# Performance work log

Measured on AMD Instinct MI355X. Metric: run time of the kernel, lower is better.

## Reference

```python
import jax, jax.numpy as jnp
import numpy as np

LEVELS = 8
DB2 = [0.4829629131445341, 0.8365163037378079, 0.22414386804185735, -0.12940952255092145]


def make_wavelet(h):
    # g = flip(h); g[1::2] *= -1  (torch compute_wavelet)
    g = jnp.flip(h, -1)
    sign = jnp.where(jnp.arange(g.shape[-1]) % 2 == 0, 1.0, -1.0).astype(g.dtype)
    return g * sign


def circ_conv(x, f, tr=False):
    # FFT-based circular convolution, output length == input length (NORM='backward').
    L = x.shape[-1]
    F = jnp.fft.rfft(f, n=L)
    if tr:
        F = jnp.conj(F)  # circular correlation for the synthesis side
    return jnp.fft.irfft(jnp.fft.rfft(x, n=L) * F, n=L)


def despawn_forward(x, scaling):
    levels = scaling.shape[0]
    L = x.shape[1]
    D = 2 ** int(np.ceil(np.log2(L)))
    pl = (D - L) // 2
    pr = int(np.ceil((D - L) / 2))
    x = jnp.pad(x, ((0, 0), (pl, pr)), mode='edge')  # ReplicationPad1d

    # Analysis: per-level circular filter + dyadic downsample
    approx = x
    details_list = []
    for lev in range(levels):
        h = scaling[lev]
        g = make_wavelet(h)
        d = circ_conv(approx, g)[:, ::2]
        approx = circ_conv(approx, h)[:, ::2]
        details_list.append(d)
    coeffs = details_list + [approx]

    # Synthesis: zero-insert upsample + circular correlation (no thresholding,
    # matching the original forward which never applies HardThreshold)
    rec = approx
    for lev in reversed(range(levels)):
        h = scaling[lev]
        g = make_wavelet(h)
        d = details_list[lev]
        n, m = d.shape
        ud = jnp.zeros((n, 2 * m), d.dtype).at[:, ::2].set(d)
        ua = jnp.zeros((n, 2 * m), rec.dtype).at[:, ::2].set(rec)
        rec = circ_conv(ud, g, tr=True) + circ_conv(ua, h, tr=True)

    return rec[:, pl:L + pr], jnp.concatenate(coeffs, axis=-1)


def setup_inputs() -> dict:
    key = jax.random.key(0)
    k1, _ = jax.random.split(key)
    x = jax.random.normal(k1, (2048, 8192), dtype=jnp.float32)
    scaling = jnp.tile(jnp.asarray(DB2, dtype=jnp.float32), (LEVELS, 1))  # (levels, 4)
    return {"x": x, "scaling": scaling}


def reference(x, scaling):
    return despawn_forward(x, scaling)
```

## Files before the change

### kernel.cpp

```cpp
#include <hip/hip_runtime.h>

#define COLS   8192
#define LEVELS 8
#define TPB    512

typedef float f4_t __attribute__((ext_vector_type(4)));

__device__ __forceinline__ void nt_store4(float* p, const float4 v) {
    f4_t w; w.x = v.x; w.y = v.y; w.z = v.z; w.w = v.w;
    __builtin_nontemporal_store(w, reinterpret_cast<f4_t*>(p));
}

__device__ __forceinline__ void bar_lds() {
    asm volatile("s_waitcnt lgkmcnt(0)" ::: "memory");
    __builtin_amdgcn_sched_barrier(0);
    __builtin_amdgcn_s_barrier();
    __builtin_amdgcn_sched_barrier(0);
}

__global__ __launch_bounds__(TPB, 8) void despawn_kernel(
    const float* __restrict__ x, const float* __restrict__ scaling,
    float* __restrict__ out, int rows)
{
    __shared__ __align__(16) float B[COLS / 2];
    __shared__ __align__(16) float C[COLS / 4];
    __shared__ __align__(16) float D[COLS / 4];
    __shared__ float filt[LEVELS * 4];

    const int row = blockIdx.x;
    const int tid = threadIdx.x;

    if (tid < LEVELS * 4) filt[tid] = scaling[tid];
    bar_lds();

    const float* __restrict__ xg       = x + (size_t)row * COLS;
    float* __restrict__       out_rec  = out + (size_t)row * COLS;
    float* __restrict__       out_coef = out + (size_t)rows * COLS + (size_t)row * COLS;

    {
        const float h0 = filt[0], h1 = filt[1], h2 = filt[2], h3 = filt[3];
        const float g0 = h3, g1 = -h2, g2 = h1, g3 = -h0;
        const float4* __restrict__ xg4 = reinterpret_cast<const float4*>(xg);
        const int q8 = COLS / 8, qm = COLS / 4 - 1;
        for (int i = tid; i < q8; i += TPB) {
            const float4 va = xg4[(2 * i - 1) & qm];
            const float4 vb = xg4[2 * i];
            const float4 vc = xg4[2 * i + 1];
            float4 dv, av;
            dv.x = g0*vb.x + g1*va.w + g2*va.z + g3*va.y;
            av.x = h0*vb.x + h1*va.w + h2*va.z + h3*va.y;
            dv.y = g0*vb.z + g1*vb.y + g2*vb.x + g3*va.w;
            av.y = h0*vb.z + h1*vb.y + h2*vb.x + h3*va.w;
            dv.z = g0*vc.x + g1*vb.w + g2*vb.z + g3*vb.y;
            av.z = h0*vc.x + h1*vb.w + h2*vb.z + h3*vb.y;
            dv.w = g0*vc.z + g1*vc.y + g2*vc.x + g3*vb.w;
            av.w = h0*vc.z + h1*vc.y + h2*vc.x + h3*vb.w;
            reinterpret_cast<float4*>(out_coef)[i] = dv;
            reinterpret_cast<float4*>(B)[i]        = av;
        }
        bar_lds();
    }

    int n = COLS / 2, coff = COLS / 2, dOff = 0;
    float* cur = B;
    float* nxt = C;
    for (int lev = 1; lev <= 3; ++lev) {
        const float h0 = filt[4*lev+0], h1 = filt[4*lev+1],
                    h2 = filt[4*lev+2], h3 = filt[4*lev+3];
        const float g0 = h3, g1 = -h2, g2 = h1, g3 = -h0;
        const int half = n >> 1, qq = half >> 2, qm = (n >> 2) - 1;
        const float4* c4 = reinterpret_cast<const float4*>(cur);
        float* ob = out_coef + coff;
        float4* n4 = reinterpret_cast<float4*>(nxt);
        float4* D4 = reinterpret_cast<float4*>(D + dOff);
        const bool toD = (lev >= 2);
        for (int p = tid; p < qq; p += TPB) {
            const float4 va = c4[(2 * p - 1) & qm];
            const float4 vb = c4[2 * p];
            const float4 vc = c4[2 * p + 1];
            float4 dv, av;
            dv.x = g0*vb.x + g1*va.w + g2*va.z + g3*va.y;
            av.x = h0*vb.x + h1*va.w + h2*va.z + h3*va.y;
            dv.y = g0*vb.z + g1*vb.y + g2*vb.x + g3*va.w;
            av.y = h0*vb.z + h1*vb.y + h2*vb.x + h3*va.w;
            dv.z = g0*vc.x + g1*vb.w + g2*vb.z + g3*vb.y;
            av.z = h0*vc.x + h1*vb.w + h2*vb.z + h3*vb.y;
            dv.w = g0*vc.z + g1*vc.y + g2*vc.x + g3*vb.w;
            av.w = h0*vc.z + h1*vc.y + h2*vc.x + h3*vb.w;
            if (toD) {
                nt_store4(ob + 4*p, dv);
                D4[p] = dv;
            } else {
                reinterpret_cast<float4*>(ob)[p] = dv;
            }
            n4[p] = av;
        }
        bar_lds();
        coff += half;
        if (toD) dOff += half;
        n = half;
        float* t = cur; cur = nxt; nxt = t;
    }

    if (tid < 64) {
        float* acur = C;
        float* anxt = B;
        int nn = 512, coffW = 7680, dW = 1536;
        for (int lev = 4; lev <= 7; ++lev) {
            const float h0 = filt[4*lev+0], h1 = filt[4*lev+1],
                        h2 = filt[4*lev+2], h3 = filt[4*lev+3];
            const float g0 = h3, g1 = -h2, g2 = h1, g3 = -h0;
            const int half = nn >> 1, mask = nn - 1;
            for (int i = tid; i < half; i += 64) {
                const int b = 2 * i;
                const float x0 = acur[b];
                const float x1 = acur[(b - 1) & mask];
                const float x2 = acur[(b - 2) & mask];
                const float x3 = acur[(b - 3) & mask];
                const float d = g0*x0 + g1*x1 + g2*x2 + g3*x3;
                const float a = h0*x0 + h1*x1 + h2*x2 + h3*x3;
                D[dW + i] = d;
                __builtin_nontemporal_store(d, &out_coef[coffW + i]);
                if (lev == 7) {
                    D[2016 + i] = a;
                    __builtin_nontemporal_store(a, &out_coef[8160 + i]);
                }
                else          anxt[i] = a;
            }
            __builtin_amdgcn_wave_barrier();
            coffW += half; dW += half; nn = half;
            float* t = acur; acur = anxt; anxt = t;
        }
        int mS = 32, dS = 1984;
        const float* aprevW = D + 2016;
        for (int lev = 7; lev >= 4; --lev) {
            const float h0 = filt[4*lev+0], h1 = filt[4*lev+1],
                        h2 = filt[4*lev+2], h3 = filt[4*lev+3];
            const float g0 = h3, g1 = -h2, g2 = h1, g3 = -h0;
            const int mm = mS - 1;
            float* recW = (lev & 1) ? B : C;
            for (int j = tid; j < mS; j += 64) {
                const float dj  = D[dS + j];
                const float dj1 = D[dS + ((j + 1) & mm)];
                const float dj2 = D[dS + ((j + 2) & mm)];
                const float aj  = aprevW[j];
                const float aj1 = aprevW[(j + 1) & mm];
                const float aj2 = aprevW[(j + 2) & mm];
                recW[2*j]     = g0*dj  + g2*dj1 + h0*aj  + h2*aj1;
                recW[2*j + 1] = g1*dj1 + g3*dj2 + h1*aj1 + h3*aj2;
            }
            __builtin_amdgcn_wave_barrier();
            aprevW = recW; mS <<= 1; dS -= mS;
        }
    }
    __syncthreads();

#define SYNTH_BODY(d2)                                                        \
    for (int p = tid; p < mp; p += TPB) {                                     \
        const float2 dv0 = (d2)[p];                                           \
        const float2 dv1 = (d2)[(p + 1) & mm];                                \
        const float2 av0 = a2[p];                                             \
        const float2 av1 = a2[(p + 1) & mm];                                  \
        const float r0 = g0*dv0.x + g2*dv0.y + h0*av0.x + h2*av0.y;           \
        const float r1 = g1*dv0.y + g3*dv1.x + h1*av0.y + h3*av1.x;           \
        const float r2 = g0*dv0.y + g2*dv1.x + h0*av0.y + h2*av1.x;           \
        const float r3 = g1*dv1.x + g3*dv1.y + h1*av1.x + h3*av1.y;           \
        const float4 rv = make_float4(r0, r1, r2, r3);                        \
        if (last) nt_store4(out_rec + 4*p, rv);                               \
        else      reinterpret_cast<float4*>(rec)[p] = rv;                     \
    }

    const float* aprev = C;
    int m = 512;
    for (int lev = 3; lev >= 0; --lev) {
        const float h0 = filt[4*lev+0], h1 = filt[4*lev+1],
                    h2 = filt[4*lev+2], h3 = filt[4*lev+3];
        const float g0 = h3, g1 = -h2, g2 = h1, g3 = -h0;
        const int mp = m >> 1, mm = mp - 1;
        const float2* a2 = reinterpret_cast<const float2*>(aprev);
        float* rec = (lev & 1) ? B : C;
        const bool last = (lev == 0);
        if (lev >= 2) {
            const float2* dL = reinterpret_cast<const float2*>(D + ((lev == 3) ? 1024 : 0));
            SYNTH_BODY(dL)
        } else {
            const float2* __restrict__ dG =
                reinterpret_cast<const float2*>(out_coef + ((lev == 1) ? 4096 : 0));
            SYNTH_BODY(dG)
        }
        if (lev) bar_lds();
        aprev = rec; m <<= 1;
    }
#undef SYNTH_BODY
}

extern "C" void kernel_launch(void* const* d_in, const int* in_sizes, int n_in,
                              void* d_out, int out_size, void* d_ws, size_t ws_size,
                              hipStream_t stream) {
    const float* x       = (const float*)d_in[0];
    const float* scaling = (const float*)d_in[1];
    float* out           = (float*)d_out;
    const int rows = in_sizes[0] / COLS;
    despawn_kernel<<<rows, TPB, 0, stream>>>(x, scaling, out, rows);
}
```

Measured before the change: 42.20 us.

## Process two rows per block and run the serial deep levels on parallel waves

Each block now handles two rows, with the shared buffers doubled per row and the grid halved. The serial single-wave stage for levels 4-7 now runs on two waves at once, one per row, so the idle tail per block is spread over more work and the barrier count per row is halved. In exchange LDS use per block doubles, the occupancy hint drops from 8 to 4, and fewer blocks are launched (1024 instead of 2048). The launch also assumes the row count is even.

```diff
diff --git a/kernel.cpp b/kernel.cpp
--- a/kernel.cpp
+++ b/kernel.cpp
@@ -3,6 +3,7 @@
 #define COLS   8192
 #define LEVELS 8
 #define TPB    512
+#define RPB    2
 
 typedef float f4_t __attribute__((ext_vector_type(4)));
 
@@ -18,180 +19,195 @@
     __builtin_amdgcn_sched_barrier(0);
 }
 
-__global__ __launch_bounds__(TPB, 8) void despawn_kernel(
+__global__ __launch_bounds__(TPB, 4) void despawn_kernel(
     const float* __restrict__ x, const float* __restrict__ scaling,
     float* __restrict__ out, int rows)
 {
-    __shared__ __align__(16) float B[COLS / 2];
-    __shared__ __align__(16) float C[COLS / 4];
-    __shared__ __align__(16) float D[COLS / 4];
+    __shared__ __align__(16) float B[RPB][4096];
+    __shared__ __align__(16) float C[RPB][2048];
+    __shared__ __align__(16) float D[RPB][2048];
     __shared__ float filt[LEVELS * 4];
 
-    const int row = blockIdx.x;
     const int tid = threadIdx.x;
-
     if (tid < LEVELS * 4) filt[tid] = scaling[tid];
     bar_lds();
 
-    const float* __restrict__ xg       = x + (size_t)row * COLS;
-    float* __restrict__       out_rec  = out + (size_t)row * COLS;
-    float* __restrict__       out_coef = out + (size_t)rows * COLS + (size_t)row * COLS;
+    const size_t row0 = (size_t)blockIdx.x * RPB;
+    const size_t cbase = (size_t)rows * COLS;
 
     {
         const float h0 = filt[0], h1 = filt[1], h2 = filt[2], h3 = filt[3];
         const float g0 = h3, g1 = -h2, g2 = h1, g3 = -h0;
-        const float4* __restrict__ xg4 = reinterpret_cast<const float4*>(xg);
         const int q8 = COLS / 8, qm = COLS / 4 - 1;
-        for (int i = tid; i < q8; i += TPB) {
-            const float4 va = xg4[(2 * i - 1) & qm];
-            const float4 vb = xg4[2 * i];
-            const float4 vc = xg4[2 * i + 1];
-            float4 dv, av;
-            dv.x = g0*vb.x + g1*va.w + g2*va.z + g3*va.y;
-            av.x = h0*vb.x + h1*va.w + h2*va.z + h3*va.y;
-            dv.y = g0*vb.z + g1*vb.y + g2*vb.x + g3*va.w;
-            av.y = h0*vb.z + h1*vb.y + h2*vb.x + h3*va.w;
-            dv.z = g0*vc.x + g1*vb.w + g2*vb.z + g3*vb.y;
-            av.z = h0*vc.x + h1*vb.w + h2*vb.z + h3*vb.y;
-            dv.w = g0*vc.z + g1*vc.y + g2*vc.x + g3*vb.w;
-            av.w = h0*vc.z + h1*vc.y + h2*vc.x + h3*vb.w;
-            reinterpret_cast<float4*>(out_coef)[i] = dv;
-            reinterpret_cast<float4*>(B)[i]        = av;
+        #pragma unroll
+        for (int r = 0; r < RPB; ++r) {
+            const float4* __restrict__ xg4 =
+                reinterpret_cast<const float4*>(x + (row0 + r) * COLS);
+            float* __restrict__ oc = out + cbase + (row0 + r) * COLS;
+            for (int i = tid; i < q8; i += TPB) {
+                const float4 va = xg4[(2 * i - 1) & qm];
+                const float4 vb = xg4[2 * i];
+                const float4 vc = xg4[2 * i + 1];
+                float4 dv, av;
+                dv.x = g0*vb.x + g1*va.w + g2*va.z + g3*va.y;
+                av.x = h0*vb.x + h1*va.w + h2*va.z + h3*va.y;
+                dv.y = g0*vb.z + g1*vb.y + g2*vb.x + g3*va.w;
+                av.y = h0*vb.z + h1*vb.y + h2*vb.x + h3*va.w;
+                dv.z = g0*vc.x + g1*vb.w + g2*vb.z + g3*vb.y;
+                av.z = h0*vc.x + h1*vb.w + h2*vb.z + h3*vb.y;
+                dv.w = g0*vc.z + g1*vc.y + g2*vc.x + g3*vb.w;
+                av.w = h0*vc.z + h1*vc.y + h2*vc.x + h3*vb.w;
+                reinterpret_cast<float4*>(oc)[i]   = dv;
+                reinterpret_cast<float4*>(B[r])[i] = av;
+            }
         }
         bar_lds();
     }
 
-    int n = COLS / 2, coff = COLS / 2, dOff = 0;
-    float* cur = B;
-    float* nxt = C;
-    for (int lev = 1; lev <= 3; ++lev) {
-        const float h0 = filt[4*lev+0], h1 = filt[4*lev+1],
-                    h2 = filt[4*lev+2], h3 = filt[4*lev+3];
-        const float g0 = h3, g1 = -h2, g2 = h1, g3 = -h0;
-        const int half = n >> 1, qq = half >> 2, qm = (n >> 2) - 1;
-        const float4* c4 = reinterpret_cast<const float4*>(cur);
-        float* ob = out_coef + coff;
-        float4* n4 = reinterpret_cast<float4*>(nxt);
-        float4* D4 = reinterpret_cast<float4*>(D + dOff);
-        const bool toD = (lev >= 2);
-        for (int p = tid; p < qq; p += TPB) {
-            const float4 va = c4[(2 * p - 1) & qm];
-            const float4 vb = c4[2 * p];
-            const float4 vc = c4[2 * p + 1];
-            float4 dv, av;
-            dv.x = g0*vb.x + g1*va.w + g2*va.z + g3*va.y;
-            av.x = h0*vb.x + h1*va.w + h2*va.z + h3*va.y;
-            dv.y = g0*vb.z + g1*vb.y + g2*vb.x + g3*va.w;
-            av.y = h0*vb.z + h1*vb.y + h2*vb.x + h3*va.w;
-            dv.z = g0*vc.x + g1*vb.w + g2*vb.z + g3*vb.y;
-            av.z = h0*vc.x + h1*vb.w + h2*vb.z + h3*vb.y;
-            dv.w = g0*vc.z + g1*vc.y + g2*vc.x + g3*vb.w;
-            av.w = h0*vc.z + h1*vc.y + h2*vc.x + h3*vb.w;
-            if (toD) {
-                nt_store4(ob + 4*p, dv);
-                D4[p] = dv;
-            } else {
-                reinterpret_cast<float4*>(ob)[p] = dv;
-            }
-            n4[p] = av;
-        }
-        bar_lds();
-        coff += half;
-        if (toD) dOff += half;
-        n = half;
-        float* t = cur; cur = nxt; nxt = t;
-    }
-
-    if (tid < 64) {
-        float* acur = C;
-        float* anxt = B;
-        int nn = 512, coffW = 7680, dW = 1536;
-        for (int lev = 4; lev <= 7; ++lev) {
+    {
+        int n = COLS / 2, coff = COLS / 2, dOff = 0;
+        float* cur[RPB] = { B[0], B[1] };
+        float* nxt[RPB] = { C[0], C[1] };
+        for (int lev = 1; lev <= 3; ++lev) {
             const float h0 = filt[4*lev+0], h1 = filt[4*lev+1],
                         h2 = filt[4*lev+2], h3 = filt[4*lev+3];
             const float g0 = h3, g1 = -h2, g2 = h1, g3 = -h0;
-            const int half = nn >> 1, mask = nn - 1;
-            for (int i = tid; i < half; i += 64) {
-                const int b = 2 * i;
-                const float x0 = acur[b];
-                const float x1 = acur[(b - 1) & mask];
-                const float x2 = acur[(b - 2) & mask];
-                const float x3 = acur[(b - 3) & mask];
-                const float d = g0*x0 + g1*x1 + g2*x2 + g3*x3;
-                const float a = h0*x0 + h1*x1 + h2*x2 + h3*x3;
-                D[dW + i] = d;
-                __builtin_nontemporal_store(d, &out_coef[coffW + i]);
-                if (lev == 7) {
-                    D[2016 + i] = a;
-                    __builtin_nontemporal_store(a, &out_coef[8160 + i]);
-                }
-                else          anxt[i] = a;
-            }
-            __builtin_amdgcn_wave_barrier();
-            coffW += half; dW += half; nn = half;
-            float* t = acur; acur = anxt; anxt = t;
-        }
-        int mS = 32, dS = 1984;
-        const float* aprevW = D + 2016;
-        for (int lev = 7; lev >= 4; --lev) {
+            const int half = n >> 1, qq = half >> 2, qm = (n >> 2) - 1;
+            const bool toD = (lev >= 2);
+            #pragma unroll
+            for (int r = 0; r < RPB; ++r) {
+                const float4* c4 = reinterpret_cast<const float4*>(cur[r]);
+                float* ob = out + cbase + (row0 + r) * COLS + coff;
+                float4* n4 = reinterpret_cast<float4*>(nxt[r]);
+                float4* D4 = reinterpret_cast<float4*>(D[r] + dOff);
+                for (int p = tid; p < qq; p += TPB) {
+                    const float4 va = c4[(2 * p - 1) & qm];
+                    const float4 vb = c4[2 * p];
+                    const float4 vc = c4[2 * p + 1];
+                    float4 dv, av;
+                    dv.x = g0*vb.x + g1*va.w + g2*va.z + g3*va.y;
+                    av.x = h0*vb.x + h1*va.w + h2*va.z + h3*va.y;
+                    dv.y = g0*vb.z + g1*vb.y + g2*vb.x + g3*va.w;
+                    av.y = h0*vb.z + h1*vb.y + h2*vb.x + h3*va.w;
+                    dv.z = g0*vc.x + g1*vb.w + g2*vb.z + g3*vb.y;
+                    av.z = h0*vc.x + h1*vb.w + h2*vb.z + h3*vb.y;
+                    dv.w = g0*vc.z + g1*vc.y + g2*vc.x + g3*vb.w;
+                    av.w = h0*vc.z + h1*vc.y + h2*vc.x + h3*vb.w;
+                    if (toD) {
+                        nt_store4(ob + 4*p, dv);
+                        D4[p] = dv;
+                    } else {
+                        reinterpret_cast<float4*>(ob)[p] = dv;
+                    }
+                    n4[p] = av;
+                }
+            }
+            bar_lds();
+            coff += half;
+            if (toD) dOff += half;
+            n = half;
+            #pragma unroll
+            for (int r = 0; r < RPB; ++r) { float* t = cur[r]; cur[r] = nxt[r]; nxt[r] = t; }
+        }
+    }
+
+    {
+        const int w = tid >> 6, lane = tid & 63;
+        if (w < RPB) {
+            const int r = w;
+            float* Br = B[r]; float* Cr = C[r]; float* Dr = D[r];
+            float* __restrict__ oc = out + cbase + (row0 + r) * COLS;
+            float* acur = Cr;
+            float* anxt = Br;
+            int nn = 512, coffW = 7680, dW = 1536;
+            for (int lev = 4; lev <= 7; ++lev) {
+                const float h0 = filt[4*lev+0], h1 = filt[4*lev+1],
+                            h2 = filt[4*lev+2], h3 = filt[4*lev+3];
+                const float g0 = h3, g1 = -h2, g2 = h1, g3 = -h0;
+                const int half = nn >> 1, mask = nn - 1;
+                for (int i = lane; i < half; i += 64) {
+                    const int b = 2 * i;
+                    const float x0 = acur[b];
+                    const float x1 = acur[(b - 1) & mask];
+                    const float x2 = acur[(b - 2) & mask];
+                    const float x3 = acur[(b - 3) & mask];
+                    const float d = g0*x0 + g1*x1 + g2*x2 + g3*x3;
+                    const float a = h0*x0 + h1*x1 + h2*x2 + h3*x3;
+                    Dr[dW + i] = d;
+                    __builtin_nontemporal_store(d, &oc[coffW + i]);
+                    if (lev == 7) {
+                        Dr[2016 + i] = a;
+                        __builtin_nontemporal_store(a, &oc[8160 + i]);
+                    }
+                    else anxt[i] = a;
+                }
+                __builtin_amdgcn_wave_barrier();
+                coffW += half; dW += half; nn = half;
+                float* t = acur; acur = anxt; anxt = t;
+            }
+            int mS = 32, dS = 1984;
+            const float* aprevW = Dr + 2016;
+            for (int lev = 7; lev >= 4; --lev) {
+                const float h0 = filt[4*lev+0], h1 = filt[4*lev+1],
+                            h2 = filt[4*lev+2], h3 = filt[4*lev+3];
+                const float g0 = h3, g1 = -h2, g2 = h1, g3 = -h0;
+                const int mm = mS - 1;
+                float* recW = (lev & 1) ? Br : Cr;
+                for (int j = lane; j < mS; j += 64) {
+                    const float dj  = Dr[dS + j];
+                    const float dj1 = Dr[dS + ((j + 1) & mm)];
+                    const float dj2 = Dr[dS + ((j + 2) & mm)];
+                    const float aj  = aprevW[j];
+                    const float aj1 = aprevW[(j + 1) & mm];
+                    const float aj2 = aprevW[(j + 2) & mm];
+                    recW[2*j]     = g0*dj  + g2*dj1 + h0*aj  + h2*aj1;
+                    recW[2*j + 1] = g1*dj1 + g3*dj2 + h1*aj1 + h3*aj2;
+                }
+                __builtin_amdgcn_wave_barrier();
+                aprevW = recW; mS <<= 1; dS -= mS;
+            }
+        }
+    }
+    __syncthreads();
+
+    {
+        const float* aprev[RPB] = { C[0], C[1] };
+        int m = 512;
+        for (int lev = 3; lev >= 0; --lev) {
             const float h0 = filt[4*lev+0], h1 = filt[4*lev+1],
                         h2 = filt[4*lev+2], h3 = filt[4*lev+3];
             const float g0 = h3, g1 = -h2, g2 = h1, g3 = -h0;
-            const int mm = mS - 1;
-            float* recW = (lev & 1) ? B : C;
-            for (int j = tid; j < mS; j += 64) {
-                const float dj  = D[dS + j];
-                const float dj1 = D[dS + ((j + 1) & mm)];
-                const float dj2 = D[dS + ((j + 2) & mm)];
-                const float aj  = aprevW[j];
-                const float aj1 = aprevW[(j + 1) & mm];
-                const float aj2 = aprevW[(j + 2) & mm];
-                recW[2*j]     = g0*dj  + g2*dj1 + h0*aj  + h2*aj1;
-                recW[2*j + 1] = g1*dj1 + g3*dj2 + h1*aj1 + h3*aj2;
-            }
-            __builtin_amdgcn_wave_barrier();
-            aprevW = recW; mS <<= 1; dS -= mS;
-        }
-    }
-    __syncthreads();
-
-#define SYNTH_BODY(d2)                                                        \
-    for (int p = tid; p < mp; p += TPB) {                                     \
-        const float2 dv0 = (d2)[p];                                           \
-        const float2 dv1 = (d2)[(p + 1) & mm];                                \
-        const float2 av0 = a2[p];                                             \
-        const float2 av1 = a2[(p + 1) & mm];                                  \
-        const float r0 = g0*dv0.x + g2*dv0.y + h0*av0.x + h2*av0.y;           \
-        const float r1 = g1*dv0.y + g3*dv1.x + h1*av0.y + h3*av1.x;           \
-        const float r2 = g0*dv0.y + g2*dv1.x + h0*av0.y + h2*av1.x;           \
-        const float r3 = g1*dv1.x + g3*dv1.y + h1*av1.x + h3*av1.y;           \
-        const float4 rv = make_float4(r0, r1, r2, r3);                        \
-        if (last) nt_store4(out_rec + 4*p, rv);                               \
-        else      reinterpret_cast<float4*>(rec)[p] = rv;                     \
-    }
-
-    const float* aprev = C;
-    int m = 512;
-    for (int lev = 3; lev >= 0; --lev) {
-        const float h0 = filt[4*lev+0], h1 = filt[4*lev+1],
-                    h2 = filt[4*lev+2], h3 = filt[4*lev+3];
-        const float g0 = h3, g1 = -h2, g2 = h1, g3 = -h0;
-        const int mp = m >> 1, mm = mp - 1;
-        const float2* a2 = reinterpret_cast<const float2*>(aprev);
-        float* rec = (lev & 1) ? B : C;
-        const bool last = (lev == 0);
-        if (lev >= 2) {
-            const float2* dL = reinterpret_cast<const float2*>(D + ((lev == 3) ? 1024 : 0));
-            SYNTH_BODY(dL)
-        } else {
-            const float2* __restrict__ dG =
-                reinterpret_cast<const float2*>(out_coef + ((lev == 1) ? 4096 : 0));
-            SYNTH_BODY(dG)
-        }
-        if (lev) bar_lds();
-        aprev = rec; m <<= 1;
-    }
-#undef SYNTH_BODY
+            const int mp = m >> 1, mm = mp - 1;
+            const bool last = (lev == 0);
+            #pragma unroll
+            for (int r = 0; r < RPB; ++r) {
+                const float2* a2 = reinterpret_cast<const float2*>(aprev[r]);
+                float* rec = (lev & 1) ? B[r] : C[r];
+                const float2* __restrict__ d2 =
+                    (lev >= 2)
+                    ? reinterpret_cast<const float2*>(D[r] + ((lev == 3) ? 1024 : 0))
+                    : reinterpret_cast<const float2*>(out + cbase + (row0 + r) * COLS
+                                                      + ((lev == 1) ? 4096 : 0));
+                float* __restrict__ orc = out + (row0 + r) * COLS;
+                for (int p = tid; p < mp; p += TPB) {
+                    const float2 dv0 = d2[p];
+                    const float2 dv1 = d2[(p + 1) & mm];
+                    const float2 av0 = a2[p];
+                    const float2 av1 = a2[(p + 1) & mm];
+                    const float r0 = g0*dv0.x + g2*dv0.y + h0*av0.x + h2*av0.y;
+                    const float r1 = g1*dv0.y + g3*dv1.x + h1*av0.y + h3*av1.x;
+                    const float r2 = g0*dv0.y + g2*dv1.x + h0*av0.y + h2*av1.x;
+                    const float r3 = g1*dv1.x + g3*dv1.y + h1*av1.x + h3*av1.y;
+                    const float4 rv = make_float4(r0, r1, r2, r3);
+                    if (last) nt_store4(orc + 4*p, rv);
+                    else      reinterpret_cast<float4*>(rec)[p] = rv;
+                }
+                aprev[r] = rec;
+            }
+            if (lev) bar_lds();
+            m <<= 1;
+        }
+    }
 }
 
 extern "C" void kernel_launch(void* const* d_in, const int* in_sizes, int n_in,
@@ -201,5 +217,5 @@
     const float* scaling = (const float*)d_in[1];
     float* out           = (float*)d_out;
     const int rows = in_sizes[0] / COLS;
-    despawn_kernel<<<rows, TPB, 0, stream>>>(x, scaling, out, rows);
-}
+    despawn_kernel<<<rows / RPB, TPB, 0, stream>>>(x, scaling, out, rows);
+}
```

Result: slower. 47.02 us (+11.4%).

## Keep deep wavelet levels in registers with wave shuffles and cache level-1 details in LDS

Applied to the files above, without the earlier changes.

The serial single-wave tail for levels 4-7 (analysis and synthesis) now runs from registers. Each lane holds 8 contiguous samples, and neighbour values are exchanged with __shfl instead of going through LDS with wave barriers. Level-1 detail coefficients are also stored in a new 16KB LDS buffer F, so synthesis level 1 reads them from LDS instead of global memory. Shared memory grows to about 46KB and the occupancy hint is dropped from launch bounds, which lowers the number of resident blocks per CU and may reduce latency hiding.

```diff
diff --git a/kernel.cpp b/kernel.cpp
--- a/kernel.cpp
+++ b/kernel.cpp
@@ -5,10 +5,15 @@
 #define TPB    512
 
 typedef float f4_t __attribute__((ext_vector_type(4)));
+typedef float f2_t __attribute__((ext_vector_type(2)));
 
 __device__ __forceinline__ void nt_store4(float* p, const float4 v) {
     f4_t w; w.x = v.x; w.y = v.y; w.z = v.z; w.w = v.w;
     __builtin_nontemporal_store(w, reinterpret_cast<f4_t*>(p));
+}
+__device__ __forceinline__ void nt_store2(float* p, float a, float b) {
+    f2_t w; w.x = a; w.y = b;
+    __builtin_nontemporal_store(w, reinterpret_cast<f2_t*>(p));
 }
 
 __device__ __forceinline__ void bar_lds() {
@@ -18,13 +23,51 @@
     __builtin_amdgcn_sched_barrier(0);
 }
 
-__global__ __launch_bounds__(TPB, 8) void despawn_kernel(
+#define ANA_LEVEL(CIN, ain, aout, dout, F0, F1, F2, F3)                       \
+    {                                                                         \
+        const int _src = (l - 1) & 63;                                        \
+        const float _m1 = __shfl(ain[(CIN)-1], _src);                         \
+        const float _m2 = __shfl(ain[(CIN)-2], _src);                         \
+        const float _m3 = __shfl(ain[(CIN)-3], _src);                         \
+        dout[0] = (F3)*ain[0] - (F2)*_m1 + (F1)*_m2 - (F0)*_m3;               \
+        aout[0] = (F0)*ain[0] + (F1)*_m1 + (F2)*_m2 + (F3)*_m3;               \
+        dout[1] = (F3)*ain[2] - (F2)*ain[1] + (F1)*ain[0] - (F0)*_m1;         \
+        aout[1] = (F0)*ain[2] + (F1)*ain[1] + (F2)*ain[0] + (F3)*_m1;         \
+        _Pragma("unroll")                                                     \
+        for (int _j = 2; _j < (CIN)/2; ++_j) {                                \
+            dout[_j] = (F3)*ain[2*_j] - (F2)*ain[2*_j-1] + (F1)*ain[2*_j-2] - (F0)*ain[2*_j-3]; \
+            aout[_j] = (F0)*ain[2*_j] + (F1)*ain[2*_j-1] + (F2)*ain[2*_j-2] + (F3)*ain[2*_j-3]; \
+        }                                                                     \
+    }
+
+#define SYN_LEVEL(CD, din, ain, rout, F0, F1, F2, F3)                         \
+    {                                                                         \
+        const int _src = (l + 1) & 63;                                        \
+        const float _d0 = __shfl(din[0], _src);                               \
+        const float _d1 = __shfl(din[1], _src);                               \
+        const float _a0 = __shfl(ain[0], _src);                               \
+        const float _a1 = __shfl(ain[1], _src);                               \
+        _Pragma("unroll")                                                     \
+        for (int _j = 0; _j < (CD); ++_j) {                                   \
+            const float dj  = din[_j];                                        \
+            const float dj1 = (_j+1 < (CD)) ? din[_j+1] : _d0;                \
+            const float dj2 = (_j+2 < (CD)) ? din[_j+2] : ((_j+1 < (CD)) ? _d0 : _d1); \
+            const float aj  = ain[_j];                                        \
+            const float aj1 = (_j+1 < (CD)) ? ain[_j+1] : _a0;                \
+            const float aj2 = (_j+2 < (CD)) ? ain[_j+2] : ((_j+1 < (CD)) ? _a0 : _a1); \
+            rout[2*_j]   = (F3)*dj + (F1)*dj1 + (F0)*aj + (F2)*aj1;           \
+            rout[2*_j+1] = -(F2)*dj1 - (F0)*dj2 + (F1)*aj1 + (F3)*aj2;        \
+        }                                                                     \
+    }
+
+__global__ __launch_bounds__(TPB) void despawn_kernel(
     const float* __restrict__ x, const float* __restrict__ scaling,
     float* __restrict__ out, int rows)
 {
-    __shared__ __align__(16) float B[COLS / 2];
-    __shared__ __align__(16) float C[COLS / 4];
-    __shared__ __align__(16) float D[COLS / 4];
+    __shared__ __align__(16) float B[4096];
+    __shared__ __align__(16) float C[2048];
+    __shared__ __align__(16) float D[1536];
+    __shared__ __align__(16) float F[4096];
     __shared__ float filt[LEVELS * 4];
 
     const int row = blockIdx.x;
@@ -61,97 +104,112 @@
         bar_lds();
     }
 
-    int n = COLS / 2, coff = COLS / 2, dOff = 0;
-    float* cur = B;
-    float* nxt = C;
-    for (int lev = 1; lev <= 3; ++lev) {
-        const float h0 = filt[4*lev+0], h1 = filt[4*lev+1],
-                    h2 = filt[4*lev+2], h3 = filt[4*lev+3];
-        const float g0 = h3, g1 = -h2, g2 = h1, g3 = -h0;
-        const int half = n >> 1, qq = half >> 2, qm = (n >> 2) - 1;
-        const float4* c4 = reinterpret_cast<const float4*>(cur);
-        float* ob = out_coef + coff;
-        float4* n4 = reinterpret_cast<float4*>(nxt);
-        float4* D4 = reinterpret_cast<float4*>(D + dOff);
-        const bool toD = (lev >= 2);
-        for (int p = tid; p < qq; p += TPB) {
-            const float4 va = c4[(2 * p - 1) & qm];
-            const float4 vb = c4[2 * p];
-            const float4 vc = c4[2 * p + 1];
-            float4 dv, av;
-            dv.x = g0*vb.x + g1*va.w + g2*va.z + g3*va.y;
-            av.x = h0*vb.x + h1*va.w + h2*va.z + h3*va.y;
-            dv.y = g0*vb.z + g1*vb.y + g2*vb.x + g3*va.w;
-            av.y = h0*vb.z + h1*vb.y + h2*vb.x + h3*va.w;
-            dv.z = g0*vc.x + g1*vb.w + g2*vb.z + g3*vb.y;
-            av.z = h0*vc.x + h1*vb.w + h2*vb.z + h3*vb.y;
-            dv.w = g0*vc.z + g1*vc.y + g2*vc.x + g3*vb.w;
-            av.w = h0*vc.z + h1*vc.y + h2*vc.x + h3*vb.w;
-            if (toD) {
-                nt_store4(ob + 4*p, dv);
-                D4[p] = dv;
-            } else {
-                reinterpret_cast<float4*>(ob)[p] = dv;
-            }
-            n4[p] = av;
-        }
-        bar_lds();
-        coff += half;
-        if (toD) dOff += half;
-        n = half;
-        float* t = cur; cur = nxt; nxt = t;
-    }
-
-    if (tid < 64) {
-        float* acur = C;
-        float* anxt = B;
-        int nn = 512, coffW = 7680, dW = 1536;
-        for (int lev = 4; lev <= 7; ++lev) {
+    {
+        int n = COLS / 2, coff = COLS / 2, dOff = 0;
+        float* cur = B;
+        float* nxt = C;
+        for (int lev = 1; lev <= 3; ++lev) {
             const float h0 = filt[4*lev+0], h1 = filt[4*lev+1],
                         h2 = filt[4*lev+2], h3 = filt[4*lev+3];
             const float g0 = h3, g1 = -h2, g2 = h1, g3 = -h0;
-            const int half = nn >> 1, mask = nn - 1;
-            for (int i = tid; i < half; i += 64) {
-                const int b = 2 * i;
-                const float x0 = acur[b];
-                const float x1 = acur[(b - 1) & mask];
-                const float x2 = acur[(b - 2) & mask];
-                const float x3 = acur[(b - 3) & mask];
-                const float d = g0*x0 + g1*x1 + g2*x2 + g3*x3;
-                const float a = h0*x0 + h1*x1 + h2*x2 + h3*x3;
-                D[dW + i] = d;
-                __builtin_nontemporal_store(d, &out_coef[coffW + i]);
-                if (lev == 7) {
-                    D[2016 + i] = a;
-                    __builtin_nontemporal_store(a, &out_coef[8160 + i]);
-                }
-                else          anxt[i] = a;
+            const int half = n >> 1, qq = half >> 2, qm = (n >> 2) - 1;
+            const float4* c4 = reinterpret_cast<const float4*>(cur);
+            float* ob = out_coef + coff;
+            float4* n4 = reinterpret_cast<float4*>(nxt);
+            float4* L4 = (lev == 1) ? reinterpret_cast<float4*>(F)
+                                    : reinterpret_cast<float4*>(D + dOff);
+            for (int p = tid; p < qq; p += TPB) {
+                const float4 va = c4[(2 * p - 1) & qm];
+                const float4 vb = c4[2 * p];
+                const float4 vc = c4[2 * p + 1];
+                float4 dv, av;
+                dv.x = g0*vb.x + g1*va.w + g2*va.z + g3*va.y;
+                av.x = h0*vb.x + h1*va.w + h2*va.z + h3*va.y;
+                dv.y = g0*vb.z + g1*vb.y + g2*vb.x + g3*va.w;
+                av.y = h0*vb.z + h1*vb.y + h2*vb.x + h3*va.w;
+                dv.z = g0*vc.x + g1*vb.w + g2*vb.z + g3*vb.y;
+                av.z = h0*vc.x + h1*vb.w + h2*vb.z + h3*vb.y;
+                dv.w = g0*vc.z + g1*vc.y + g2*vc.x + g3*vb.w;
+                av.w = h0*vc.z + h1*vc.y + h2*vc.x + h3*vb.w;
+                nt_store4(ob + 4*p, dv);
+                L4[p] = dv;
+                n4[p] = av;
             }
-            __builtin_amdgcn_wave_barrier();
-            coffW += half; dW += half; nn = half;
-            float* t = acur; acur = anxt; anxt = t;
-        }
-        int mS = 32, dS = 1984;
-        const float* aprevW = D + 2016;
-        for (int lev = 7; lev >= 4; --lev) {
-            const float h0 = filt[4*lev+0], h1 = filt[4*lev+1],
-                        h2 = filt[4*lev+2], h3 = filt[4*lev+3];
-            const float g0 = h3, g1 = -h2, g2 = h1, g3 = -h0;
-            const int mm = mS - 1;
-            float* recW = (lev & 1) ? B : C;
-            for (int j = tid; j < mS; j += 64) {
-                const float dj  = D[dS + j];
-                const float dj1 = D[dS + ((j + 1) & mm)];
-                const float dj2 = D[dS + ((j + 2) & mm)];
-                const float aj  = aprevW[j];
-                const float aj1 = aprevW[(j + 1) & mm];
-                const float aj2 = aprevW[(j + 2) & mm];
-                recW[2*j]     = g0*dj  + g2*dj1 + h0*aj  + h2*aj1;
-                recW[2*j + 1] = g1*dj1 + g3*dj2 + h1*aj1 + h3*aj2;
-            }
-            __builtin_amdgcn_wave_barrier();
-            aprevW = recW; mS <<= 1; dS -= mS;
-        }
+            bar_lds();
+            coff += half;
+            if (lev >= 2) dOff += half;
+            n = half;
+            float* t = cur; cur = nxt; nxt = t;
+        }
+    }
+
+    if (tid < 64) {
+        const int l = tid;
+        float a3r[8];
+        {
+            const float4 v0 = reinterpret_cast<const float4*>(C)[2*l];
+            const float4 v1 = reinterpret_cast<const float4*>(C)[2*l+1];
+            a3r[0]=v0.x; a3r[1]=v0.y; a3r[2]=v0.z; a3r[3]=v0.w;
+            a3r[4]=v1.x; a3r[5]=v1.y; a3r[6]=v1.z; a3r[7]=v1.w;
+        }
+        float a4r[4], d4r[4];
+        ANA_LEVEL(8, a3r, a4r, d4r, filt[16], filt[17], filt[18], filt[19]);
+        float a5r[2], d5r[2];
+        ANA_LEVEL(4, a4r, a5r, d5r, filt[20], filt[21], filt[22], filt[23]);
+        float a6r, d6r;
+        {
+            const float F0=filt[24],F1=filt[25],F2=filt[26],F3=filt[27];
+            const int s1 = (l-1)&63, s2 = (l-2)&63;
+            const float x0 = a5r[0];
+            const float x1 = __shfl(a5r[1], s1);
+            const float x2 = __shfl(a5r[0], s1);
+            const float x3 = __shfl(a5r[1], s2);
+            d6r = F3*x0 - F2*x1 + F1*x2 - F0*x3;
+            a6r = F0*x0 + F1*x1 + F2*x2 + F3*x3;
+        }
+        float d7r, apr;
+        {
+            const float F0=filt[28],F1=filt[29],F2=filt[30],F3=filt[31];
+            const int i2 = 2*l;
+            const float x0 = __shfl(a6r, i2 & 63);
+            const float x1 = __shfl(a6r, (i2-1)&63);
+            const float x2 = __shfl(a6r, (i2-2)&63);
+            const float x3 = __shfl(a6r, (i2-3)&63);
+            d7r = F3*x0 - F2*x1 + F1*x2 - F0*x3;
+            apr = F0*x0 + F1*x1 + F2*x2 + F3*x3;
+        }
+        nt_store4(out_coef + 7680 + 4*l, make_float4(d4r[0],d4r[1],d4r[2],d4r[3]));
+        nt_store2(out_coef + 7936 + 2*l, d5r[0], d5r[1]);
+        __builtin_nontemporal_store(d6r, &out_coef[8064 + l]);
+        if (l < 32) {
+            __builtin_nontemporal_store(d7r, &out_coef[8128 + l]);
+            __builtin_nontemporal_store(apr, &out_coef[8160 + l]);
+        }
+        float rec7;
+        {
+            const float F0=filt[28],F1=filt[29],F2=filt[30],F3=filt[31];
+            const float dj = d7r, dj1 = __shfl(d7r,(l+1)&31), dj2 = __shfl(d7r,(l+2)&31);
+            const float aj = apr, aj1 = __shfl(apr,(l+1)&31), aj2 = __shfl(apr,(l+2)&31);
+            const float r0 = F3*dj + F1*dj1 + F0*aj + F2*aj1;
+            const float r1 = -F2*dj1 - F0*dj2 + F1*aj1 + F3*aj2;
+            const float e0 = __shfl(r0, l>>1);
+            const float e1 = __shfl(r1, l>>1);
+            rec7 = (l & 1) ? e1 : e0;
+        }
+        float rec6[2];
+        {
+            const float F0=filt[24],F1=filt[25],F2=filt[26],F3=filt[27];
+            const float dj = d6r, dj1 = __shfl(d6r,(l+1)&63), dj2 = __shfl(d6r,(l+2)&63);
+            const float aj = rec7, aj1 = __shfl(rec7,(l+1)&63), aj2 = __shfl(rec7,(l+2)&63);
+            rec6[0] = F3*dj + F1*dj1 + F0*aj + F2*aj1;
+            rec6[1] = -F2*dj1 - F0*dj2 + F1*aj1 + F3*aj2;
+        }
+        float rec5[4];
+        SYN_LEVEL(2, d5r, rec6, rec5, filt[20], filt[21], filt[22], filt[23]);
+        float rec4r[8];
+        SYN_LEVEL(4, d4r, rec5, rec4r, filt[16], filt[17], filt[18], filt[19]);
+        reinterpret_cast<float4*>(C)[2*l]   = make_float4(rec4r[0],rec4r[1],rec4r[2],rec4r[3]);
+        reinterpret_cast<float4*>(C)[2*l+1] = make_float4(rec4r[4],rec4r[5],rec4r[6],rec4r[7]);
     }
     __syncthreads();
 
@@ -183,9 +241,11 @@
         if (lev >= 2) {
             const float2* dL = reinterpret_cast<const float2*>(D + ((lev == 3) ? 1024 : 0));
             SYNTH_BODY(dL)
+        } else if (lev == 1) {
+            const float2* dF = reinterpret_cast<const float2*>(F);
+            SYNTH_BODY(dF)
         } else {
-            const float2* __restrict__ dG =
-                reinterpret_cast<const float2*>(out_coef + ((lev == 1) ? 4096 : 0));
+            const float2* __restrict__ dG = reinterpret_cast<const float2*>(out_coef);
             SYNTH_BODY(dG)
         }
         if (lev) bar_lds();
```

New measurement: 42.57 us. No clear change (+0.9%).

## Prefetch global detail coefficients into registers before synthesis levels

Applied to the files above, without the earlier changes.

Unrolls the four synthesis levels explicitly and issues the global loads of level-0 and level-1 detail coefficients into registers before the LDS-based levels 3 and 2 run. This overlaps global-memory (likely L2) latency with earlier synthesis work instead of stalling at each level. It also drops the occupancy hint from launch bounds, which lets the compiler use more registers for the prefetched values at the risk of lower occupancy.

```diff
diff --git a/kernel.cpp b/kernel.cpp
--- a/kernel.cpp
+++ b/kernel.cpp
@@ -18,7 +18,7 @@
     __builtin_amdgcn_sched_barrier(0);
 }
 
-__global__ __launch_bounds__(TPB, 8) void despawn_kernel(
+__global__ __launch_bounds__(TPB) void despawn_kernel(
     const float* __restrict__ x, const float* __restrict__ scaling,
     float* __restrict__ out, int rows)
 {
@@ -155,43 +155,95 @@
     }
     __syncthreads();
 
-#define SYNTH_BODY(d2)                                                        \
-    for (int p = tid; p < mp; p += TPB) {                                     \
-        const float2 dv0 = (d2)[p];                                           \
-        const float2 dv1 = (d2)[(p + 1) & mm];                                \
-        const float2 av0 = a2[p];                                             \
-        const float2 av1 = a2[(p + 1) & mm];                                  \
-        const float r0 = g0*dv0.x + g2*dv0.y + h0*av0.x + h2*av0.y;           \
-        const float r1 = g1*dv0.y + g3*dv1.x + h1*av0.y + h3*av1.x;           \
-        const float r2 = g0*dv0.y + g2*dv1.x + h0*av0.y + h2*av1.x;           \
-        const float r3 = g1*dv1.x + g3*dv1.y + h1*av1.x + h3*av1.y;           \
-        const float4 rv = make_float4(r0, r1, r2, r3);                        \
-        if (last) nt_store4(out_rec + 4*p, rv);                               \
-        else      reinterpret_cast<float4*>(rec)[p] = rv;                     \
-    }
-
-    const float* aprev = C;
-    int m = 512;
-    for (int lev = 3; lev >= 0; --lev) {
-        const float h0 = filt[4*lev+0], h1 = filt[4*lev+1],
-                    h2 = filt[4*lev+2], h3 = filt[4*lev+3];
-        const float g0 = h3, g1 = -h2, g2 = h1, g3 = -h0;
-        const int mp = m >> 1, mm = mp - 1;
-        const float2* a2 = reinterpret_cast<const float2*>(aprev);
-        float* rec = (lev & 1) ? B : C;
-        const bool last = (lev == 0);
-        if (lev >= 2) {
-            const float2* dL = reinterpret_cast<const float2*>(D + ((lev == 3) ? 1024 : 0));
-            SYNTH_BODY(dL)
-        } else {
-            const float2* __restrict__ dG =
-                reinterpret_cast<const float2*>(out_coef + ((lev == 1) ? 4096 : 0));
-            SYNTH_BODY(dG)
-        }
-        if (lev) bar_lds();
-        aprev = rec; m <<= 1;
-    }
-#undef SYNTH_BODY
+    const float2* __restrict__ d1g = reinterpret_cast<const float2*>(out_coef + 4096);
+    const float2* __restrict__ d0g = reinterpret_cast<const float2*>(out_coef);
+    float2 pf1a[2], pf1b[2], pf0a[4], pf0b[4];
+    #pragma unroll
+    for (int i = 0; i < 2; ++i) {
+        const int p = tid + i * TPB;
+        pf1a[i] = d1g[p];
+        pf1b[i] = d1g[(p + 1) & 1023];
+    }
+    #pragma unroll
+    for (int i = 0; i < 4; ++i) {
+        const int p = tid + i * TPB;
+        pf0a[i] = d0g[p];
+        pf0b[i] = d0g[(p + 1) & 2047];
+    }
+
+    {
+        const float h0=filt[12],h1=filt[13],h2=filt[14],h3=filt[15];
+        const float g0=h3,g1=-h2,g2=h1,g3=-h0;
+        const float2* dL = reinterpret_cast<const float2*>(D + 1024);
+        const float2* a2 = reinterpret_cast<const float2*>(C);
+        for (int p = tid; p < 256; p += TPB) {
+            const float2 dv0 = dL[p];
+            const float2 dv1 = dL[(p + 1) & 255];
+            const float2 av0 = a2[p];
+            const float2 av1 = a2[(p + 1) & 255];
+            const float r0 = g0*dv0.x + g2*dv0.y + h0*av0.x + h2*av0.y;
+            const float r1 = g1*dv0.y + g3*dv1.x + h1*av0.y + h3*av1.x;
+            const float r2 = g0*dv0.y + g2*dv1.x + h0*av0.y + h2*av1.x;
+            const float r3 = g1*dv1.x + g3*dv1.y + h1*av1.x + h3*av1.y;
+            reinterpret_cast<float4*>(B)[p] = make_float4(r0, r1, r2, r3);
+        }
+        bar_lds();
+    }
+    {
+        const float h0=filt[8],h1=filt[9],h2=filt[10],h3=filt[11];
+        const float g0=h3,g1=-h2,g2=h1,g3=-h0;
+        const float2* dL = reinterpret_cast<const float2*>(D);
+        const float2* a2 = reinterpret_cast<const float2*>(B);
+        for (int p = tid; p < 512; p += TPB) {
+            const float2 dv0 = dL[p];
+            const float2 dv1 = dL[(p + 1) & 511];
+            const float2 av0 = a2[p];
+            const float2 av1 = a2[(p + 1) & 511];
+            const float r0 = g0*dv0.x + g2*dv0.y + h0*av0.x + h2*av0.y;
+            const float r1 = g1*dv0.y + g3*dv1.x + h1*av0.y + h3*av1.x;
+            const float r2 = g0*dv0.y + g2*dv1.x + h0*av0.y + h2*av1.x;
+            const float r3 = g1*dv1.x + g3*dv1.y + h1*av1.x + h3*av1.y;
+            reinterpret_cast<float4*>(C)[p] = make_float4(r0, r1, r2, r3);
+        }
+        bar_lds();
+    }
+    {
+        const float h0=filt[4],h1=filt[5],h2=filt[6],h3=filt[7];
+        const float g0=h3,g1=-h2,g2=h1,g3=-h0;
+        const float2* a2 = reinterpret_cast<const float2*>(C);
+        #pragma unroll
+        for (int i = 0; i < 2; ++i) {
+            const int p = tid + i * TPB;
+            const float2 dv0 = pf1a[i];
+            const float2 dv1 = pf1b[i];
+            const float2 av0 = a2[p];
+            const float2 av1 = a2[(p + 1) & 1023];
+            const float r0 = g0*dv0.x + g2*dv0.y + h0*av0.x + h2*av0.y;
+            const float r1 = g1*dv0.y + g3*dv1.x + h1*av0.y + h3*av1.x;
+            const float r2 = g0*dv0.y + g2*dv1.x + h0*av0.y + h2*av1.x;
+            const float r3 = g1*dv1.x + g3*dv1.y + h1*av1.x + h3*av1.y;
+            reinterpret_cast<float4*>(B)[p] = make_float4(r0, r1, r2, r3);
+        }
+        bar_lds();
+    }
+    {
+        const float h0=filt[0],h1=filt[1],h2=filt[2],h3=filt[3];
+        const float g0=h3,g1=-h2,g2=h1,g3=-h0;
+        const float2* a2 = reinterpret_cast<const float2*>(B);
+        #pragma unroll
+        for (int i = 0; i < 4; ++i) {
+            const int p = tid + i * TPB;
+            const float2 dv0 = pf0a[i];
+            const float2 dv1 = pf0b[i];
+            const float2 av0 = a2[p];
+            const float2 av1 = a2[(p + 1) & 2047];
+            const float r0 = g0*dv0.x + g2*dv0.y + h0*av0.x + h2*av0.y;
+            const float r1 = g1*dv0.y + g3*dv1.x + h1*av0.y + h3*av1.x;
+            const float r2 = g0*dv0.y + g2*dv1.x + h0*av0.y + h2*av1.x;
+            const float r3 = g1*dv1.x + g3*dv1.y + h1*av1.x + h3*av1.y;
+            nt_store4(out_rec + 4*p, make_float4(r0, r1, r2, r3));
+        }
+    }
 }
 
 extern "C" void kernel_launch(void* const* d_in, const int* in_sizes, int n_in,
```

Result: no change. 42.57 us (+0.9%).
